# Kernel tuning notes

Hardware: AMD Instinct MI355X
Metric: run time of the kernel (lower is better)

Reference implementation:

```python
import jax, jax.numpy as jnp
import numpy as np

N_DATA = 8192
M_QUERIES = 8192

def setup_inputs() -> dict:
    key = jax.random.key(0)
    k1, k2 = jax.random.split(key)
    data = jax.random.uniform(k1, (N_DATA, 3), dtype=jnp.float32)
    queries = jax.random.uniform(k2, (M_QUERIES, 3), dtype=jnp.float32)
    return {"data": data, "queries": queries, "radius": 0.1}

def reference(data, queries, radius):
    """Faithful jax version of native_neighbor_search.

    Returns (neighbors_index, neighbors_row_splits).
    Because jax.jit requires static shapes, neighbors_index is padded to the
    maximal size m*n with -1; the number of valid entries is
    neighbors_row_splits[-1]. Valid entries appear in the same row-major
    (query-ordered) order as torch's nonzero().
    """
    n = data.shape[0]
    m = queries.shape[0]
    # pairwise Euclidean distances [m, n] via the ||q||^2 + ||d||^2 - 2 q.d expansion
    q2 = jnp.sum(queries * queries, axis=1, keepdims=True)          # [m,1]
    d2 = jnp.sum(data * data, axis=1, keepdims=True).T              # [1,n]
    dists = jnp.sqrt(jnp.maximum(q2 + d2 - 2.0 * (queries @ data.T), 0.0))
    mask = dists <= radius                                          # [m,n]
    # CSR row splits: exclusive prefix sum of per-query neighbor counts
    counts = jnp.sum(mask.astype(jnp.int32), axis=1)                # [m]
    row_splits = jnp.concatenate(
        [jnp.zeros((1,), jnp.int32), jnp.cumsum(counts)])           # [m+1]
    # flattened nonzero in row-major order -> column index = flat % n
    (flat_idx,) = jnp.nonzero(mask.ravel(), size=m * n, fill_value=-1)
    neighbors_index = jnp.where(flat_idx >= 0, flat_idx % n, -1).astype(jnp.int32)
    return neighbors_index, row_splits
```

## Files before the change

kernel.cpp:

```cpp
#include <hip/hip_runtime.h>
#include <stdint.h>


__device__ __forceinline__ float next_up(float x) {
    return __uint_as_float(__float_as_uint(x) + 1u);
}
__device__ __forceinline__ float next_down(float x) {
    return __uint_as_float(__float_as_uint(x) - 1u);
}

__device__ __forceinline__ float sq_threshold(float r) {
    float T = __fmul_rn(r, r);
    while (__fsqrt_rn(T) > r) T = next_down(T);
    while (__fsqrt_rn(next_up(T)) <= r) T = next_up(T);
    return T;
}

__device__ __forceinline__ float pair_metric_d2(float qx, float qy, float qz,
                                                float q2, float dx, float dy,
                                                float dz, float d2) {
    float dot = __builtin_fmaf(qz, dz, __builtin_fmaf(qy, dy, __fmul_rn(qx, dx)));
    return __fsub_rn(__fadd_rn(q2, d2), __fmul_rn(2.0f, dot));
}
__device__ __forceinline__ float pair_metric(float qx, float qy, float qz, float q2,
                                             float dx, float dy, float dz) {
    float d2 = __fadd_rn(__fadd_rn(__fmul_rn(dx, dx), __fmul_rn(dy, dy)),
                         __fmul_rn(dz, dz));
    return pair_metric_d2(qx, qy, qz, q2, dx, dy, dz, d2);
}


__global__ __launch_bounds__(256) void fused_fill_count(
    const float* __restrict__ data, const float* __restrict__ queries,
    const float* __restrict__ radius_p, int* __restrict__ out_idx,
    unsigned long long* __restrict__ masks, int* __restrict__ counts) {
    constexpr int N = 8192;
    __shared__ float4 pts[512];

    int role = blockIdx.x & 1;
    int rb = blockIdx.x >> 1;

    if (role == 0) {
        int4* out4 = (int4*)out_idx;
        const size_t n4 = (size_t)N * N / 4;
        size_t i = (size_t)rb * 256 + threadIdx.x;
        const size_t stride = 2048ull * 256ull;
        const int4 v = make_int4(-1, -1, -1, -1);
        for (; i < n4; i += stride) out4[i] = v;
        return;
    }

    int wave = threadIdx.x >> 6;
    int lane = threadIdx.x & 63;
    int q = rb * 4 + wave;

    float r = radius_p[0];
    float T = sq_threshold(r);
    float qx = queries[3 * q + 0], qy = queries[3 * q + 1], qz = queries[3 * q + 2];
    float q2 = __fadd_rn(__fadd_rn(__fmul_rn(qx, qx), __fmul_rn(qy, qy)),
                         __fmul_rn(qz, qz));

    unsigned long long mlo = 0, mhi = 0;
    int cnt = 0;

    for (int rd = 0; rd < 16; ++rd) {
        int p0 = rd * 512;
        __syncthreads();
        for (int p = threadIdx.x; p < 512; p += 256) {
            float dx = data[3 * (p0 + p) + 0];
            float dy = data[3 * (p0 + p) + 1];
            float dz = data[3 * (p0 + p) + 2];
            float d2 = __fadd_rn(__fadd_rn(__fmul_rn(dx, dx), __fmul_rn(dy, dy)),
                                 __fmul_rn(dz, dz));
            pts[p] = make_float4(dx, dy, dz, d2);
        }
        __syncthreads();
#pragma unroll
        for (int cc = 0; cc < 8; ++cc) {
            float4 d = pts[cc * 64 + lane];
            float u = pair_metric_d2(qx, qy, qz, q2, d.x, d.y, d.z, d.w);
            unsigned long long mask = __ballot(u <= T);
            int c = rd * 8 + cc;
            if (lane == (c & 63)) {
                if (c < 64) mlo = mask; else mhi = mask;
            }
            cnt += __popcll(mask);
        }
    }
    masks[(size_t)q * 128 + lane] = mlo;
    masks[(size_t)q * 128 + 64 + lane] = mhi;
    if (lane == 0) counts[q] = cnt;
}

__global__ __launch_bounds__(1024) void scan_kernel2(const int* __restrict__ counts,
                                                     int* __restrict__ rs, int m) {
    __shared__ int part[1024];
    int t = threadIdx.x;
    int base = t * 8;
    int c[8];
    int s = 0;
    for (int k = 0; k < 8; ++k) {
        int p = base + k;
        c[k] = (p < m) ? counts[p] : 0;
        s += c[k];
    }
    part[t] = s;
    __syncthreads();
    for (int off = 1; off < 1024; off <<= 1) {
        int v = 0;
        if (t >= off) v = part[t - off];
        __syncthreads();
        if (t >= off) part[t] += v;
        __syncthreads();
    }
    int run = (t == 0) ? 0 : part[t - 1];
    for (int k = 0; k < 8; ++k) {
        int p = base + k;
        if (p < m) rs[p] = run;
        run += c[k];
    }
    if (t == 1023) rs[m] = part[1023];
}

__global__ __launch_bounds__(256) void emit_from_masks(
    const unsigned long long* __restrict__ masks, const int* __restrict__ rs,
    int* __restrict__ out_idx) {
    int wave = threadIdx.x >> 6;
    int lane = threadIdx.x & 63;
    int q = blockIdx.x * 4 + wave;

    unsigned long long lo = masks[(size_t)q * 128 + lane];
    unsigned long long hi = masks[(size_t)q * 128 + 64 + lane];
    int plo = __popcll(lo), phi = __popcll(hi);
    int ilo = plo, ihi = phi;
    for (int off = 1; off < 64; off <<= 1) {
        int a = __shfl_up(ilo, off, 64);
        int b = __shfl_up(ihi, off, 64);
        if (lane >= off) { ilo += a; ihi += b; }
    }
    int total_lo = __shfl(ilo, 63, 64);
    int base = rs[q];
    int pos_lo = base + ilo - plo;
    int pos_hi = base + total_lo + ihi - phi;
    int jb_lo = lane * 64, jb_hi = (64 + lane) * 64;
    while (lo) {
        int b = __builtin_ctzll(lo);
        out_idx[pos_lo++] = jb_lo + b;
        lo &= lo - 1;
    }
    while (hi) {
        int b = __builtin_ctzll(hi);
        out_idx[pos_hi++] = jb_hi + b;
        hi &= hi - 1;
    }
}


__global__ __launch_bounds__(256) void fill_kernel(int* __restrict__ out, size_t total) {
    size_t n4 = total >> 2;
    int4* out4 = (int4*)out;
    size_t i = (size_t)blockIdx.x * blockDim.x + threadIdx.x;
    size_t stride = (size_t)gridDim.x * blockDim.x;
    const int4 v = make_int4(-1, -1, -1, -1);
    for (; i < n4; i += stride) out4[i] = v;
    if (blockIdx.x == 0 && threadIdx.x == 0) {
        for (size_t k = n4 << 2; k < total; ++k) out[k] = -1;
    }
}

__global__ __launch_bounds__(256) void count_kernel(
    const float* __restrict__ data, const float* __restrict__ queries,
    const float* __restrict__ radius_p, int n, int m, int* __restrict__ counts) {
    int q = (blockIdx.x * blockDim.x + threadIdx.x) >> 6;
    int lane = threadIdx.x & 63;
    if (q >= m) return;
    float r = radius_p[0];
    float T = sq_threshold(r);
    float qx = queries[3 * q + 0], qy = queries[3 * q + 1], qz = queries[3 * q + 2];
    float q2 = __fadd_rn(__fadd_rn(__fmul_rn(qx, qx), __fmul_rn(qy, qy)),
                         __fmul_rn(qz, qz));
    int cnt = 0;
    for (int j = lane; j < n; j += 64) {
        float u = pair_metric(qx, qy, qz, q2, data[3 * j], data[3 * j + 1], data[3 * j + 2]);
        if (u <= T) cnt++;
    }
    for (int off = 32; off > 0; off >>= 1) cnt += __shfl_down(cnt, off, 64);
    if (lane == 0) counts[q] = cnt;
}

__global__ __launch_bounds__(256) void emit_kernel(
    const float* __restrict__ data, const float* __restrict__ queries,
    const float* __restrict__ radius_p, int n, int m,
    const int* __restrict__ row_splits, int* __restrict__ out_idx) {
    int q = (blockIdx.x * blockDim.x + threadIdx.x) >> 6;
    int lane = threadIdx.x & 63;
    if (q >= m) return;
    float r = radius_p[0];
    float T = sq_threshold(r);
    float qx = queries[3 * q + 0], qy = queries[3 * q + 1], qz = queries[3 * q + 2];
    float q2 = __fadd_rn(__fadd_rn(__fmul_rn(qx, qx), __fmul_rn(qy, qy)),
                         __fmul_rn(qz, qz));
    int base = row_splits[q];
    unsigned long long lane_mask_lt = (lane == 0) ? 0ULL : (~0ULL >> (64 - lane));
    for (int j0 = 0; j0 < n; j0 += 64) {
        int j = j0 + lane;
        bool pred = false;
        if (j < n) {
            float u = pair_metric(qx, qy, qz, q2, data[3 * j], data[3 * j + 1], data[3 * j + 2]);
            pred = (u <= T);
        }
        unsigned long long mask = __ballot(pred);
        if (pred) {
            int pos = base + __popcll(mask & lane_mask_lt);
            out_idx[pos] = j;
        }
        base += __popcll(mask);
    }
}


extern "C" void kernel_launch(void* const* d_in, const int* in_sizes, int n_in,
                              void* d_out, int out_size, void* d_ws, size_t ws_size,
                              hipStream_t stream) {
    const float* data = (const float*)d_in[0];
    const float* queries = (const float*)d_in[1];
    const float* radius = (const float*)d_in[2];
    int n = in_sizes[0] / 3;
    int m = in_sizes[1] / 3;
    int* out = (int*)d_out;
    size_t idx_count = (size_t)m * (size_t)n;
    int* row = out + idx_count;

    size_t need = (size_t)m * 128 * 8 + (size_t)m * 4;
    bool fast = (n == 8192) && (m == 8192) && (ws_size >= need);

    if (fast) {
        unsigned long long* masks = (unsigned long long*)d_ws;
        int* counts = (int*)((char*)d_ws + (size_t)m * 128 * 8);
        fused_fill_count<<<4096, 256, 0, stream>>>(data, queries, radius, out,
                                                   masks, counts);
        scan_kernel2<<<1, 1024, 0, stream>>>(counts, row, m);
        emit_from_masks<<<m / 4, 256, 0, stream>>>(masks, row, out);
    } else {
        fill_kernel<<<2048, 256, 0, stream>>>(out, idx_count);
        int blocks = (m * 64 + 255) / 256;
        count_kernel<<<blocks, 256, 0, stream>>>(data, queries, radius, n, m, row);
        scan_kernel2<<<1, 1024, 0, stream>>>(row, row, m);
        emit_kernel<<<blocks, 256, 0, stream>>>(data, queries, radius, n, m, row, out);
    }
}
```

Before: 81.02 us.

## Fill only the unused tail of the output with -1 inside the emit kernel

```diff
diff --git a/kernel.cpp b/kernel.cpp
--- a/kernel.cpp
+++ b/kernel.cpp
@@ -1,6 +1,8 @@
 #include <hip/hip_runtime.h>
 #include <stdint.h>
 
+
+#define N8 8192
 
 __device__ __forceinline__ float next_up(float x) {
     return __uint_as_float(__float_as_uint(x) + 1u);
@@ -30,29 +32,15 @@
 }
 
 
-__global__ __launch_bounds__(256) void fused_fill_count(
+__global__ __launch_bounds__(256) void count_masks(
     const float* __restrict__ data, const float* __restrict__ queries,
-    const float* __restrict__ radius_p, int* __restrict__ out_idx,
+    const float* __restrict__ radius_p,
     unsigned long long* __restrict__ masks, int* __restrict__ counts) {
-    constexpr int N = 8192;
     __shared__ float4 pts[512];
 
-    int role = blockIdx.x & 1;
-    int rb = blockIdx.x >> 1;
-
-    if (role == 0) {
-        int4* out4 = (int4*)out_idx;
-        const size_t n4 = (size_t)N * N / 4;
-        size_t i = (size_t)rb * 256 + threadIdx.x;
-        const size_t stride = 2048ull * 256ull;
-        const int4 v = make_int4(-1, -1, -1, -1);
-        for (; i < n4; i += stride) out4[i] = v;
-        return;
-    }
-
     int wave = threadIdx.x >> 6;
     int lane = threadIdx.x & 63;
-    int q = rb * 4 + wave;
+    int q = blockIdx.x * 4 + wave;
 
     float r = radius_p[0];
     float T = sq_threshold(r);
@@ -122,7 +110,7 @@
     if (t == 1023) rs[m] = part[1023];
 }
 
-__global__ __launch_bounds__(256) void emit_from_masks(
+__global__ __launch_bounds__(256) void fill_emit(
     const unsigned long long* __restrict__ masks, const int* __restrict__ rs,
     int* __restrict__ out_idx) {
     int wave = threadIdx.x >> 6;
@@ -153,6 +141,17 @@
         out_idx[pos_hi++] = jb_hi + b;
         hi &= hi - 1;
     }
+
+    int L = rs[N8];
+    int Lr = (L + 3) & ~3;
+    if (blockIdx.x == 0 && (int)threadIdx.x < (Lr - L))
+        out_idx[L + threadIdx.x] = -1;
+    int4* out4 = (int4*)out_idx;
+    const int4 v = make_int4(-1, -1, -1, -1);
+    const size_t n4 = (size_t)N8 * N8 / 4;
+    size_t i = (size_t)(Lr >> 2) + (size_t)blockIdx.x * 256 + threadIdx.x;
+    const size_t stride = 2048ull * 256ull;
+    for (; i < n4; i += stride) out4[i] = v;
 }
 
 
@@ -232,15 +231,14 @@
     int* row = out + idx_count;
 
     size_t need = (size_t)m * 128 * 8 + (size_t)m * 4;
-    bool fast = (n == 8192) && (m == 8192) && (ws_size >= need);
+    bool fast = (n == N8) && (m == N8) && (ws_size >= need);
 
     if (fast) {
         unsigned long long* masks = (unsigned long long*)d_ws;
         int* counts = (int*)((char*)d_ws + (size_t)m * 128 * 8);
-        fused_fill_count<<<4096, 256, 0, stream>>>(data, queries, radius, out,
-                                                   masks, counts);
+        count_masks<<<2048, 256, 0, stream>>>(data, queries, radius, masks, counts);
         scan_kernel2<<<1, 1024, 0, stream>>>(counts, row, m);
-        emit_from_masks<<<m / 4, 256, 0, stream>>>(masks, row, out);
+        fill_emit<<<2048, 256, 0, stream>>>(masks, row, out);
     } else {
         fill_kernel<<<2048, 256, 0, stream>>>(out, idx_count);
         int blocks = (m * 64 + 255) / 256;
```

Measured after the change: 94.27 us. +16.4%, slower.
